# Kernel optimization log

Hardware: AMD Instinct MI355X
Metric: run time of the kernel (lower is better)

The kernel has to match this reference:

```python
import jax, jax.numpy as jnp
import numpy as np

B, T, C, H = 2, 2048, 1024, 16
HD = C // H  # 64

def setup_inputs() -> dict:
    key = jax.random.key(0)
    ks = jax.random.split(key, 9)
    s = 0.02
    return {
        "x": jax.random.normal(ks[0], (B, T, C), jnp.float32),
        "Wq": jax.random.normal(ks[1], (C, C), jnp.float32) * s,
        "bq": jax.random.normal(ks[2], (C,), jnp.float32) * s,
        "Wk": jax.random.normal(ks[3], (C, C), jnp.float32) * s,
        "bk": jax.random.normal(ks[4], (C,), jnp.float32) * s,
        "Wv": jax.random.normal(ks[5], (C, C), jnp.float32) * s,
        "bv": jax.random.normal(ks[6], (C,), jnp.float32) * s,
        "Wp": jax.random.normal(ks[7], (C, C), jnp.float32) * s,
        "bp": jax.random.normal(ks[8], (C,), jnp.float32) * s,
    }

def reference(x, Wq, bq, Wk, bk, Wv, bv, Wp, bp):
    Bb, Tt, Cc = x.shape
    hd = Cc // H
    # project and split heads: [B, H, T, hd]
    def heads(W, b):
        return (x @ W.T + b).reshape(Bb, Tt, H, hd).transpose(0, 2, 1, 3)
    q, k, v = heads(Wq, bq), heads(Wk, bk), heads(Wv, bv)
    scale = 1.0 / np.sqrt(hd).astype(np.float32)
    att = jnp.einsum('bhqd,bhkd->bhqk', q, k) * scale
    causal = jnp.tril(jnp.ones((Tt, Tt), bool))
    att = jnp.where(causal[None, None], att, -jnp.inf)
    att = jax.nn.softmax(att, axis=-1)
    y = jnp.einsum('bhqk,bhkd->bhqd', att, v)
    y = y.transpose(0, 2, 1, 3).reshape(Bb, Tt, Cc)
    return y @ Wp.T + bp
```

## Files before the change

kernel.cpp:

```cpp
#include <hip/hip_runtime.h>
#include <hip/hip_bf16.h>

#define Tsz 2048
#define Csz 1024
#define Hn 16

typedef short s8v __attribute__((ext_vector_type(8)));
typedef short s4v __attribute__((ext_vector_type(4)));
typedef float f4v __attribute__((ext_vector_type(4)));
typedef int   i4v __attribute__((ext_vector_type(4)));
typedef unsigned u2v __attribute__((ext_vector_type(2)));

#define QSCALE (0.125f * 1.44269504088896f)

__device__ __forceinline__ unsigned short bfr(float x) {
    return (unsigned short)((__builtin_bit_cast(unsigned, x) + 0x8000u) >> 16);
}
__device__ __forceinline__ unsigned pack2_rn(float a, float b) {
    const unsigned ua = __builtin_bit_cast(unsigned, a) + 0x8000u;
    const unsigned ub = __builtin_bit_cast(unsigned, b) + 0x8000u;
    return (ua >> 16) | (ub & 0xFFFF0000u);
}
__device__ __forceinline__ unsigned cvt2(float a, float b) {
    __hip_bfloat162 h = __float22bfloat162_rn(float2{a, b});
    unsigned r;
    __builtin_memcpy(&r, &h, 4);
    return r;
}

__device__ __forceinline__ void gload_lds(const void* g, void* l) {
    __builtin_amdgcn_global_load_lds(
        (const __attribute__((address_space(1))) void*)g,
        (__attribute__((address_space(3))) void*)l, 16, 0, 0);
}

__global__ void cvt6(const float* __restrict__ x, const float* __restrict__ wq,
                     const float* __restrict__ wk, const float* __restrict__ wv,
                     const float* __restrict__ wp,
                     short* __restrict__ xo, short* __restrict__ qo,
                     short* __restrict__ ko, short* __restrict__ vo,
                     short* __restrict__ po) {
    const int bx = blockIdx.x;
    const float* in; short* out; int ib;
    if (bx < 4096) { in = x; out = xo; ib = bx; }
    else {
        const int r = bx - 4096, w = r >> 10;
        ib = r & 1023;
        switch (w) {
            case 0: in = wq; out = qo; break;
            case 1: in = wk; out = ko; break;
            case 2: in = wv; out = vo; break;
            default: in = wp; out = po; break;
        }
    }
    const int i = ib * 1024 + threadIdx.x * 4;
    float4 v = *(const float4*)(in + i);
    int2 o;
    o.x = (int)pack2_rn(v.x, v.y);
    o.y = (int)pack2_rn(v.z, v.w);
    *(int2*)(out + i) = o;
}

__global__ __launch_bounds__(256, 3) void qkv_gemm(
    const short* __restrict__ X,
    const short* __restrict__ Wq, const short* __restrict__ Wk, const short* __restrict__ Wv,
    const float* __restrict__ bq, const float* __restrict__ bk, const float* __restrict__ bv,
    short* __restrict__ Qo, short* __restrict__ Ko, short* __restrict__ Vto)
{
    const int z = blockIdx.z;
    const short* W = (z == 0) ? Wq : (z == 1) ? Wk : Wv;
    const float* bias = (z == 0) ? bq : (z == 1) ? bk : bv;

    __shared__ __align__(16) short Ash[128 * 32];
    __shared__ __align__(16) short Bsh[128 * 32];
    __shared__ __align__(16) short TR[64 * 72];

    const int tid = threadIdx.x, lane = tid & 63, wave = tid >> 6;
    const int ln = lane & 15, hi = lane >> 4;
    const int m0 = blockIdx.x * 128, n0 = blockIdx.y * 128;
    const int wm = (wave >> 1) * 64, wn = (wave & 1) * 64;

    const short* Ag = X + (size_t)(m0 + (tid >> 2)) * Csz + (tid & 3) * 8;
    const short* Bg = W + (size_t)(n0 + (tid >> 2)) * Csz + (tid & 3) * 8;

    f4v acc[4][4];
    #pragma unroll
    for (int mt = 0; mt < 4; mt++)
        #pragma unroll
        for (int nt = 0; nt < 4; nt++)
            #pragma unroll
            for (int i = 0; i < 4; i++) acc[mt][nt][i] = 0.f;

    for (int k0 = 0; k0 < Csz; k0 += 32) {
        __syncthreads();
        gload_lds(Ag + k0, Ash + tid * 8);
        gload_lds(Ag + k0 + (size_t)64 * Csz, Ash + 2048 + tid * 8);
        gload_lds(Bg + k0, Bsh + tid * 8);
        gload_lds(Bg + k0 + (size_t)64 * Csz, Bsh + 2048 + tid * 8);
        __syncthreads();

        s8v af[4], bfr_[4];
        #pragma unroll
        for (int mt = 0; mt < 4; mt++)
            af[mt] = *(const s8v*)(Ash + (wm + mt * 16 + ln) * 32 + hi * 8);
        #pragma unroll
        for (int nt = 0; nt < 4; nt++)
            bfr_[nt] = *(const s8v*)(Bsh + (wn + nt * 16 + ln) * 32 + hi * 8);
        #pragma unroll
        for (int mt = 0; mt < 4; mt++)
            #pragma unroll
            for (int nt = 0; nt < 4; nt++)
                acc[mt][nt] = __builtin_amdgcn_mfma_f32_16x16x32_bf16(af[mt], bfr_[nt], acc[mt][nt], 0, 0, 0);
    }

    if (z == 2) {
        const int b = m0 >> 11, t0 = m0 & 2047;
        float bvv[4];
        #pragma unroll
        for (int nt = 0; nt < 4; nt++) bvv[nt] = bias[n0 + wn + nt * 16 + ln];
        #pragma unroll
        for (int ph = 0; ph < 4; ph++) {
            const int mh = ph >> 1, nh = ph & 1;
            __syncthreads();
            if ((wave >> 1) == mh && (wave & 1) == nh) {
                #pragma unroll
                for (int mt = 0; mt < 4; mt++)
                    #pragma unroll
                    for (int nt = 0; nt < 4; nt++) {
                        int2 pk;
                        pk.x = (int)pack2_rn(acc[mt][nt][0] + bvv[nt], acc[mt][nt][1] + bvv[nt]);
                        pk.y = (int)pack2_rn(acc[mt][nt][2] + bvv[nt], acc[mt][nt][3] + bvv[nt]);
                        *(int2*)(TR + (nt * 16 + ln) * 72 + mt * 16 + hi * 4) = pk;
                    }
            }
            __syncthreads();
            const int chl = tid >> 2, seg = tid & 3;
            const s8v r0 = *(const s8v*)(TR + chl * 72 + seg * 16);
            const s8v r1 = *(const s8v*)(TR + chl * 72 + seg * 16 + 8);
            short* dst = Vto + (size_t)(b * 1024 + n0 + nh * 64 + chl) * Tsz + t0 + mh * 64 + seg * 16;
            *(s8v*)(dst) = r0;
            *(s8v*)(dst + 8) = r1;
        }
        return;
    }

    const float scale = (z == 0) ? QSCALE : 1.0f;
    short* out = (z == 0) ? Qo : Ko;

    #pragma unroll
    for (int nt = 0; nt < 4; nt++) {
        const int col = n0 + wn + nt * 16 + ln;
        const float bvv = bias[col];
        #pragma unroll
        for (int mt = 0; mt < 4; mt++) {
            const int row0 = m0 + wm + mt * 16 + hi * 4;
            #pragma unroll
            for (int i = 0; i < 4; i++)
                out[(size_t)(row0 + i) * Csz + col] = (short)bfr((acc[mt][nt][i] + bvv) * scale);
        }
    }
}

__global__ __launch_bounds__(256, 2) void proj_gemm(
    const short* __restrict__ A, const short* __restrict__ W,
    const float* __restrict__ bias, float* __restrict__ out)
{
    __shared__ __align__(16) short Ash[128 * 32];
    __shared__ __align__(16) short Bsh[64 * 32];

    const int tid = threadIdx.x, lane = tid & 63, wave = tid >> 6;
    const int ln = lane & 15, hi = lane >> 4;
    const int m0 = blockIdx.x * 128, n0 = blockIdx.y * 64;
    const int wm = (wave >> 1) * 64, wn = (wave & 1) * 32;

    const short* Ag = A + (size_t)(m0 + (tid >> 2)) * Csz + (tid & 3) * 8;
    const short* Bg = W + (size_t)(n0 + (tid >> 2)) * Csz + (tid & 3) * 8;

    f4v acc[4][2];
    #pragma unroll
    for (int mt = 0; mt < 4; mt++)
        #pragma unroll
        for (int nt = 0; nt < 2; nt++)
            #pragma unroll
            for (int i = 0; i < 4; i++) acc[mt][nt][i] = 0.f;

    for (int k0 = 0; k0 < Csz; k0 += 32) {
        __syncthreads();
        gload_lds(Ag + k0, Ash + tid * 8);
        gload_lds(Ag + k0 + (size_t)64 * Csz, Ash + 2048 + tid * 8);
        gload_lds(Bg + k0, Bsh + tid * 8);
        __syncthreads();

        s8v af[4], bfr_[2];
        #pragma unroll
        for (int mt = 0; mt < 4; mt++)
            af[mt] = *(const s8v*)(Ash + (wm + mt * 16 + ln) * 32 + hi * 8);
        #pragma unroll
        for (int nt = 0; nt < 2; nt++)
            bfr_[nt] = *(const s8v*)(Bsh + (wn + nt * 16 + ln) * 32 + hi * 8);
        #pragma unroll
        for (int mt = 0; mt < 4; mt++)
            #pragma unroll
            for (int nt = 0; nt < 2; nt++)
                acc[mt][nt] = __builtin_amdgcn_mfma_f32_16x16x32_bf16(af[mt], bfr_[nt], acc[mt][nt], 0, 0, 0);
    }

    #pragma unroll
    for (int nt = 0; nt < 2; nt++) {
        const int col = n0 + wn + nt * 16 + ln;
        const float bvv = bias[col];
        #pragma unroll
        for (int mt = 0; mt < 4; mt++)
            #pragma unroll
            for (int i = 0; i < 4; i++)
                out[(size_t)(m0 + wm + mt * 16 + hi * 4 + i) * Csz + col] = acc[mt][nt][i] + bvv;
    }
}

__global__ __launch_bounds__(256, 3) void attn16(
    const short* __restrict__ Q, const short* __restrict__ Kg,
    const short* __restrict__ Vt, short* __restrict__ Y)
{
    __shared__ __align__(16) short SB[3][2][64 * 64];

    const int tid = threadIdx.x, lane = tid & 63, wave = tid >> 6;
    const int ln = lane & 15, hi = lane >> 4;

    const int n = blockIdx.x;
    const int c = n & 255, j = n >> 8;
    const int bh = (j << 3) | (c >> 5);
    const int t = c & 31;
    const int qt = (j & 1) ? t : 31 - t;

    const size_t base = (size_t)(bh >> 4) * Tsz * Csz + (size_t)(bh & 15) * 64;
    const size_t vtbase = (size_t)bh * 64 * Tsz;
    const int qrel = wave * 16 + ln;

    s8v qf[2];
    #pragma unroll
    for (int kk = 0; kk < 2; kk++)
        qf[kk] = *(const s8v*)(Q + base + (size_t)(qt * 64 + qrel) * Csz + kk * 32 + hi * 8);

    f4v o[4];
    f4v lacc;
    #pragma unroll
    for (int i = 0; i < 4; i++) lacc[i] = 0.f;
    #pragma unroll
    for (int dt = 0; dt < 4; dt++)
        #pragma unroll
        for (int i = 0; i < 4; i++) o[dt][i] = 0.f;

    const s8v ones8 = { (short)0x3F80, (short)0x3F80, (short)0x3F80, (short)0x3F80,
                        (short)0x3F80, (short)0x3F80, (short)0x3F80, (short)0x3F80 };

    const int sr = tid >> 3, scs = tid & 7;
    const int csw = (scs ^ (sr & 7)) * 8;
    const short* KsA = Kg + base + (size_t)sr * Csz + csw;
    const short* KsB = KsA + (size_t)32 * Csz;
    const short* VsA = Vt + vtbase + (size_t)sr * Tsz + csw;
    const short* VsB = VsA + (size_t)32 * Tsz;
    const int nkb = qt + 1;

    int foff[2][4];
    #pragma unroll
    for (int nt = 0; nt < 4; nt++)
        #pragma unroll
        for (int kk = 0; kk < 2; kk++)
            foff[kk][nt] = (nt * 16 + ln) * 64 + (((kk * 4 + hi) ^ (ln & 7)) * 8);

    #define STAGE3(B) {                                    \
        gload_lds(KsA, &SB[B][0][tid * 8]);                \
        gload_lds(KsB, &SB[B][0][2048 + tid * 8]);         \
        gload_lds(VsA, &SB[B][1][tid * 8]);                \
        gload_lds(VsB, &SB[B][1][2048 + tid * 8]);         \
        KsA += (size_t)64 * Csz; KsB += (size_t)64 * Csz;  \
        VsA += 64; VsB += 64;                              \
    }

    STAGE3(0);
    if (nkb > 1) {
        STAGE3(1);
        asm volatile("s_waitcnt vmcnt(4)" ::: "memory");
    } else {
        asm volatile("s_waitcnt vmcnt(0)" ::: "memory");
    }
    __builtin_amdgcn_s_barrier();

    #define TILE(B0, B2, kb_) {                                                     \
        const bool st_ = (kb_) + 2 < nkb;                                           \
        if (st_) STAGE3(B2);                                                        \
        s8v kf[2][4], vf[2][4];                                                     \
        for (int nt = 0; nt < 4; nt++) {                                            \
            kf[0][nt] = *(const s8v*)(&SB[B0][0][foff[0][nt]]);                     \
            kf[1][nt] = *(const s8v*)(&SB[B0][0][foff[1][nt]]);                     \
            vf[0][nt] = *(const s8v*)(&SB[B0][1][foff[0][nt]]);                     \
            vf[1][nt] = *(const s8v*)(&SB[B0][1][foff[1][nt]]);                     \
        }                                                                           \
        f4v s[4];                                                                   \
        for (int nt = 0; nt < 4; nt++) {                                            \
            for (int i = 0; i < 4; i++) s[nt][i] = 0.f;                             \
            s[nt] = __builtin_amdgcn_mfma_f32_16x16x32_bf16(kf[0][nt], qf[0], s[nt], 0, 0, 0); \
            s[nt] = __builtin_amdgcn_mfma_f32_16x16x32_bf16(kf[1][nt], qf[1], s[nt], 0, 0, 0); \
        }                                                                           \
        const bool dg_ = ((kb_) == qt);                                             \
        unsigned pw[4][2];                                                          \
        for (int nt = 0; nt < 4; nt++) {                                            \
            float e0 = exp2f(s[nt][0]), e1 = exp2f(s[nt][1]);                       \
            float e2 = exp2f(s[nt][2]), e3 = exp2f(s[nt][3]);                       \
            if (dg_) {                                                              \
                const int kr = nt * 16 + hi * 4;                                    \
                if (kr + 0 > qrel) e0 = 0.f;                                        \
                if (kr + 1 > qrel) e1 = 0.f;                                        \
                if (kr + 2 > qrel) e2 = 0.f;                                        \
                if (kr + 3 > qrel) e3 = 0.f;                                        \
            }                                                                       \
            pw[nt][0] = cvt2(e0, e1);                                               \
            pw[nt][1] = cvt2(e2, e3);                                               \
        }                                                                           \
        u2v r0a = __builtin_amdgcn_permlane32_swap(pw[0][0], pw[1][0], false, false); \
        u2v r0b = __builtin_amdgcn_permlane16_swap(r0a[0], r0a[1], false, false);   \
        u2v r1a = __builtin_amdgcn_permlane32_swap(pw[0][1], pw[1][1], false, false); \
        u2v r1b = __builtin_amdgcn_permlane16_swap(r1a[0], r1a[1], false, false);   \
        u2v r2a = __builtin_amdgcn_permlane32_swap(pw[2][0], pw[3][0], false, false); \
        u2v r2b = __builtin_amdgcn_permlane16_swap(r2a[0], r2a[1], false, false);   \
        u2v r3a = __builtin_amdgcn_permlane32_swap(pw[2][1], pw[3][1], false, false); \
        u2v r3b = __builtin_amdgcn_permlane16_swap(r3a[0], r3a[1], false, false);   \
        i4v p0 = { (int)r0b[0], (int)r1b[0], (int)r0b[1], (int)r1b[1] };            \
        i4v p1 = { (int)r2b[0], (int)r3b[0], (int)r2b[1], (int)r3b[1] };            \
        const s8v pb0 = __builtin_bit_cast(s8v, p0);                                \
        const s8v pb1 = __builtin_bit_cast(s8v, p1);                                \
        for (int dt = 0; dt < 4; dt++) {                                            \
            o[dt] = __builtin_amdgcn_mfma_f32_16x16x32_bf16(vf[0][dt], pb0, o[dt], 0, 0, 0); \
            o[dt] = __builtin_amdgcn_mfma_f32_16x16x32_bf16(vf[1][dt], pb1, o[dt], 0, 0, 0); \
        }                                                                           \
        lacc = __builtin_amdgcn_mfma_f32_16x16x32_bf16(ones8, pb0, lacc, 0, 0, 0);  \
        lacc = __builtin_amdgcn_mfma_f32_16x16x32_bf16(ones8, pb1, lacc, 0, 0, 0);  \
        if ((kb_) + 1 < nkb) {                                                      \
            if (st_) asm volatile("s_waitcnt vmcnt(4)" ::: "memory");               \
            else     asm volatile("s_waitcnt vmcnt(0)" ::: "memory");               \
            __builtin_amdgcn_s_barrier();                                           \
        }                                                                           \
    }

    for (int kb = 0; kb < nkb; kb += 3) {
        TILE(0, 2, kb);
        if (kb + 1 < nkb) TILE(1, 0, kb + 1);
        if (kb + 2 < nkb) TILE(2, 1, kb + 2);
    }
    #undef TILE
    #undef STAGE3

    const float inv = 1.0f / lacc[0];
    const int qrow = qt * 64 + qrel;
    #pragma unroll
    for (int dt = 0; dt < 4; dt++) {
        int2 w;
        w.x = (int)cvt2(o[dt][0] * inv, o[dt][1] * inv);
        w.y = (int)cvt2(o[dt][2] * inv, o[dt][3] * inv);
        *(int2*)(Y + base + (size_t)qrow * Csz + dt * 16 + hi * 4) = w;
    }
}

extern "C" void kernel_launch(void* const* d_in, const int* in_sizes, int n_in,
                              void* d_out, int out_size, void* d_ws, size_t ws_size,
                              hipStream_t stream) {
    const float* x  = (const float*)d_in[0];
    const float* Wq = (const float*)d_in[1];
    const float* bq = (const float*)d_in[2];
    const float* Wk = (const float*)d_in[3];
    const float* bk = (const float*)d_in[4];
    const float* Wv = (const float*)d_in[5];
    const float* bv = (const float*)d_in[6];
    const float* Wp = (const float*)d_in[7];
    const float* bp = (const float*)d_in[8];

    char* ws = (char*)d_ws;
    short* Xb  = (short*)(ws);
    short* Wqb = (short*)(ws + (8u  << 20));
    short* Wkb = (short*)(ws + (10u << 20));
    short* Wvb = (short*)(ws + (12u << 20));
    short* Wpb = (short*)(ws + (14u << 20));
    short* Qb  = (short*)(ws + (16u << 20));
    short* Kb  = (short*)(ws + (24u << 20));
    short* Vtb = (short*)(ws + (32u << 20));
    short* Yb  = (short*)(ws + (40u << 20));

    hipLaunchKernelGGL(cvt6, dim3(8192), dim3(256), 0, stream,
                       x, Wq, Wk, Wv, Wp, Xb, Wqb, Wkb, Wvb, Wpb);

    hipLaunchKernelGGL(qkv_gemm, dim3(32, 8, 3), dim3(256), 0, stream,
                       Xb, Wqb, Wkb, Wvb, bq, bk, bv, Qb, Kb, Vtb);

    hipLaunchKernelGGL(attn16, dim3(1024), dim3(256), 0, stream, Qb, Kb, Vtb, Yb);

    hipLaunchKernelGGL(proj_gemm, dim3(32, 16), dim3(256), 0, stream, Yb, Wpb, bp, (float*)d_out);
}
```

Baseline: 187.3 us.

## Pair causal query tiles per block to balance work and share K/V loads

Each attention block now handles two query tiles, t and 31-t, so every block processes the same 33 key tiles and shares each staged K/V tile between both queries. The grid drops from 1024 to 512 blocks. Pipelining goes from triple to double buffering with a full vmcnt(0) wait per tile, and launch bounds fall to 2 blocks per CU. This trades less prefetch depth, higher register pressure and lower occupancy for balanced work per block and fewer K/V loads.

New measurement: 178.8 us (median of 2 runs). 1.05x faster.

```diff
diff --git a/kernel.cpp b/kernel.cpp
--- a/kernel.cpp
+++ b/kernel.cpp
@@ -217,38 +217,44 @@
     }
 }
 
-__global__ __launch_bounds__(256, 3) void attn16(
+__global__ __launch_bounds__(256, 2) void attn17(
     const short* __restrict__ Q, const short* __restrict__ Kg,
     const short* __restrict__ Vt, short* __restrict__ Y)
 {
-    __shared__ __align__(16) short SB[3][2][64 * 64];
+    __shared__ __align__(16) short SB[2][2][64 * 64];
 
     const int tid = threadIdx.x, lane = tid & 63, wave = tid >> 6;
     const int ln = lane & 15, hi = lane >> 4;
 
     const int n = blockIdx.x;
-    const int c = n & 255, j = n >> 8;
-    const int bh = (j << 3) | (c >> 5);
-    const int t = c & 31;
-    const int qt = (j & 1) ? t : 31 - t;
+    const int j = n >> 8, n0 = n & 255;
+    const int bh = n0 >> 3, ti = n0 & 7;
+    const int t = j ? (15 - ti) : ti;
+    const int qts_[2] = { t, 31 - t };
+    const int nkb = 32 - t;
 
     const size_t base = (size_t)(bh >> 4) * Tsz * Csz + (size_t)(bh & 15) * 64;
     const size_t vtbase = (size_t)bh * 64 * Tsz;
     const int qrel = wave * 16 + ln;
 
-    s8v qf[2];
-    #pragma unroll
-    for (int kk = 0; kk < 2; kk++)
-        qf[kk] = *(const s8v*)(Q + base + (size_t)(qt * 64 + qrel) * Csz + kk * 32 + hi * 8);
-
-    f4v o[4];
-    f4v lacc;
-    #pragma unroll
-    for (int i = 0; i < 4; i++) lacc[i] = 0.f;
-    #pragma unroll
-    for (int dt = 0; dt < 4; dt++)
-        #pragma unroll
-        for (int i = 0; i < 4; i++) o[dt][i] = 0.f;
+    s8v qf[2][2];
+    #pragma unroll
+    for (int tt = 0; tt < 2; tt++)
+        #pragma unroll
+        for (int kk = 0; kk < 2; kk++)
+            qf[tt][kk] = *(const s8v*)(Q + base + (size_t)(qts_[tt] * 64 + qrel) * Csz + kk * 32 + hi * 8);
+
+    f4v o[2][4];
+    f4v lacc[2];
+    #pragma unroll
+    for (int tt = 0; tt < 2; tt++) {
+        #pragma unroll
+        for (int i = 0; i < 4; i++) lacc[tt][i] = 0.f;
+        #pragma unroll
+        for (int dt = 0; dt < 4; dt++)
+            #pragma unroll
+            for (int i = 0; i < 4; i++) o[tt][dt][i] = 0.f;
+    }
 
     const s8v ones8 = { (short)0x3F80, (short)0x3F80, (short)0x3F80, (short)0x3F80,
                         (short)0x3F80, (short)0x3F80, (short)0x3F80, (short)0x3F80 };
@@ -259,7 +265,6 @@
     const short* KsB = KsA + (size_t)32 * Csz;
     const short* VsA = Vt + vtbase + (size_t)sr * Tsz + csw;
     const short* VsB = VsA + (size_t)32 * Tsz;
-    const int nkb = qt + 1;
 
     int foff[2][4];
     #pragma unroll
@@ -268,27 +273,21 @@
         for (int kk = 0; kk < 2; kk++)
             foff[kk][nt] = (nt * 16 + ln) * 64 + (((kk * 4 + hi) ^ (ln & 7)) * 8);
 
-    #define STAGE3(B) {                                    \
-        gload_lds(KsA, &SB[B][0][tid * 8]);                \
-        gload_lds(KsB, &SB[B][0][2048 + tid * 8]);         \
-        gload_lds(VsA, &SB[B][1][tid * 8]);                \
-        gload_lds(VsB, &SB[B][1][2048 + tid * 8]);         \
-        KsA += (size_t)64 * Csz; KsB += (size_t)64 * Csz;  \
-        VsA += 64; VsB += 64;                              \
-    }
-
-    STAGE3(0);
-    if (nkb > 1) {
-        STAGE3(1);
-        asm volatile("s_waitcnt vmcnt(4)" ::: "memory");
-    } else {
-        asm volatile("s_waitcnt vmcnt(0)" ::: "memory");
-    }
+    #define STAGE(B, kb_) {                                      \
+        const size_t ko_ = (size_t)(kb_) * 64;                   \
+        gload_lds(KsA + ko_ * Csz, &SB[B][0][tid * 8]);          \
+        gload_lds(KsB + ko_ * Csz, &SB[B][0][2048 + tid * 8]);   \
+        gload_lds(VsA + ko_,       &SB[B][1][tid * 8]);          \
+        gload_lds(VsB + ko_,       &SB[B][1][2048 + tid * 8]);   \
+    }
+
+    STAGE(0, 0);
+    asm volatile("s_waitcnt vmcnt(0)" ::: "memory");
     __builtin_amdgcn_s_barrier();
 
-    #define TILE(B0, B2, kb_) {                                                     \
-        const bool st_ = (kb_) + 2 < nkb;                                           \
-        if (st_) STAGE3(B2);                                                        \
+    #define TILE(B0, B1, kb_) {                                                     \
+        const bool st_ = (kb_) + 1 < nkb;                                           \
+        if (st_) STAGE(B1, (kb_) + 1);                                              \
         s8v kf[2][4], vf[2][4];                                                     \
         for (int nt = 0; nt < 4; nt++) {                                            \
             kf[0][nt] = *(const s8v*)(&SB[B0][0][foff[0][nt]]);                     \
@@ -296,68 +295,73 @@
             vf[0][nt] = *(const s8v*)(&SB[B0][1][foff[0][nt]]);                     \
             vf[1][nt] = *(const s8v*)(&SB[B0][1][foff[1][nt]]);                     \
         }                                                                           \
-        f4v s[4];                                                                   \
-        for (int nt = 0; nt < 4; nt++) {                                            \
-            for (int i = 0; i < 4; i++) s[nt][i] = 0.f;                             \
-            s[nt] = __builtin_amdgcn_mfma_f32_16x16x32_bf16(kf[0][nt], qf[0], s[nt], 0, 0, 0); \
-            s[nt] = __builtin_amdgcn_mfma_f32_16x16x32_bf16(kf[1][nt], qf[1], s[nt], 0, 0, 0); \
+        _Pragma("unroll")                                                           \
+        for (int tt = 0; tt < 2; tt++) {                                            \
+            if ((kb_) > qts_[tt]) continue;                       \
+            f4v s[4];                                                               \
+            for (int nt = 0; nt < 4; nt++) {                                        \
+                for (int i = 0; i < 4; i++) s[nt][i] = 0.f;                         \
+                s[nt] = __builtin_amdgcn_mfma_f32_16x16x32_bf16(kf[0][nt], qf[tt][0], s[nt], 0, 0, 0); \
+                s[nt] = __builtin_amdgcn_mfma_f32_16x16x32_bf16(kf[1][nt], qf[tt][1], s[nt], 0, 0, 0); \
+            }                                                                       \
+            const bool dg_ = ((kb_) == qts_[tt]);                                   \
+            unsigned pw[4][2];                                                      \
+            for (int nt = 0; nt < 4; nt++) {                                        \
+                float e0 = exp2f(s[nt][0]), e1 = exp2f(s[nt][1]);                   \
+                float e2 = exp2f(s[nt][2]), e3 = exp2f(s[nt][3]);                   \
+                if (dg_) {                                                          \
+                    const int kr = nt * 16 + hi * 4;                                \
+                    if (kr + 0 > qrel) e0 = 0.f;                                    \
+                    if (kr + 1 > qrel) e1 = 0.f;                                    \
+                    if (kr + 2 > qrel) e2 = 0.f;                                    \
+                    if (kr + 3 > qrel) e3 = 0.f;                                    \
+                }                                                                   \
+                pw[nt][0] = cvt2(e0, e1);                                           \
+                pw[nt][1] = cvt2(e2, e3);                                           \
+            }                                                                       \
+            u2v r0a = __builtin_amdgcn_permlane32_swap(pw[0][0], pw[1][0], false, false); \
+            u2v r0b = __builtin_amdgcn_permlane16_swap(r0a[0], r0a[1], false, false); \
+            u2v r1a = __builtin_amdgcn_permlane32_swap(pw[0][1], pw[1][1], false, false); \
+            u2v r1b = __builtin_amdgcn_permlane16_swap(r1a[0], r1a[1], false, false); \
+            u2v r2a = __builtin_amdgcn_permlane32_swap(pw[2][0], pw[3][0], false, false); \
+            u2v r2b = __builtin_amdgcn_permlane16_swap(r2a[0], r2a[1], false, false); \
+            u2v r3a = __builtin_amdgcn_permlane32_swap(pw[2][1], pw[3][1], false, false); \
+            u2v r3b = __builtin_amdgcn_permlane16_swap(r3a[0], r3a[1], false, false); \
+            i4v p0 = { (int)r0b[0], (int)r1b[0], (int)r0b[1], (int)r1b[1] };        \
+            i4v p1 = { (int)r2b[0], (int)r3b[0], (int)r2b[1], (int)r3b[1] };        \
+            const s8v pb0 = __builtin_bit_cast(s8v, p0);                            \
+            const s8v pb1 = __builtin_bit_cast(s8v, p1);                            \
+            for (int dt = 0; dt < 4; dt++) {                                        \
+                o[tt][dt] = __builtin_amdgcn_mfma_f32_16x16x32_bf16(vf[0][dt], pb0, o[tt][dt], 0, 0, 0); \
+                o[tt][dt] = __builtin_amdgcn_mfma_f32_16x16x32_bf16(vf[1][dt], pb1, o[tt][dt], 0, 0, 0); \
+            }                                                                       \
+            lacc[tt] = __builtin_amdgcn_mfma_f32_16x16x32_bf16(ones8, pb0, lacc[tt], 0, 0, 0); \
+            lacc[tt] = __builtin_amdgcn_mfma_f32_16x16x32_bf16(ones8, pb1, lacc[tt], 0, 0, 0); \
         }                                                                           \
-        const bool dg_ = ((kb_) == qt);                                             \
-        unsigned pw[4][2];                                                          \
-        for (int nt = 0; nt < 4; nt++) {                                            \
-            float e0 = exp2f(s[nt][0]), e1 = exp2f(s[nt][1]);                       \
-            float e2 = exp2f(s[nt][2]), e3 = exp2f(s[nt][3]);                       \
-            if (dg_) {                                                              \
-                const int kr = nt * 16 + hi * 4;                                    \
-                if (kr + 0 > qrel) e0 = 0.f;                                        \
-                if (kr + 1 > qrel) e1 = 0.f;                                        \
-                if (kr + 2 > qrel) e2 = 0.f;                                        \
-                if (kr + 3 > qrel) e3 = 0.f;                                        \
-            }                                                                       \
-            pw[nt][0] = cvt2(e0, e1);                                               \
-            pw[nt][1] = cvt2(e2, e3);                                               \
-        }                                                                           \
-        u2v r0a = __builtin_amdgcn_permlane32_swap(pw[0][0], pw[1][0], false, false); \
-        u2v r0b = __builtin_amdgcn_permlane16_swap(r0a[0], r0a[1], false, false);   \
-        u2v r1a = __builtin_amdgcn_permlane32_swap(pw[0][1], pw[1][1], false, false); \
-        u2v r1b = __builtin_amdgcn_permlane16_swap(r1a[0], r1a[1], false, false);   \
-        u2v r2a = __builtin_amdgcn_permlane32_swap(pw[2][0], pw[3][0], false, false); \
-        u2v r2b = __builtin_amdgcn_permlane16_swap(r2a[0], r2a[1], false, false);   \
-        u2v r3a = __builtin_amdgcn_permlane32_swap(pw[2][1], pw[3][1], false, false); \
-        u2v r3b = __builtin_amdgcn_permlane16_swap(r3a[0], r3a[1], false, false);   \
-        i4v p0 = { (int)r0b[0], (int)r1b[0], (int)r0b[1], (int)r1b[1] };            \
-        i4v p1 = { (int)r2b[0], (int)r3b[0], (int)r2b[1], (int)r3b[1] };            \
-        const s8v pb0 = __builtin_bit_cast(s8v, p0);                                \
-        const s8v pb1 = __builtin_bit_cast(s8v, p1);                                \
-        for (int dt = 0; dt < 4; dt++) {                                            \
-            o[dt] = __builtin_amdgcn_mfma_f32_16x16x32_bf16(vf[0][dt], pb0, o[dt], 0, 0, 0); \
-            o[dt] = __builtin_amdgcn_mfma_f32_16x16x32_bf16(vf[1][dt], pb1, o[dt], 0, 0, 0); \
-        }                                                                           \
-        lacc = __builtin_amdgcn_mfma_f32_16x16x32_bf16(ones8, pb0, lacc, 0, 0, 0);  \
-        lacc = __builtin_amdgcn_mfma_f32_16x16x32_bf16(ones8, pb1, lacc, 0, 0, 0);  \
-        if ((kb_) + 1 < nkb) {                                                      \
-            if (st_) asm volatile("s_waitcnt vmcnt(4)" ::: "memory");               \
-            else     asm volatile("s_waitcnt vmcnt(0)" ::: "memory");               \
+        if (st_) {                                                                  \
+            asm volatile("s_waitcnt vmcnt(0)" ::: "memory");                        \
             __builtin_amdgcn_s_barrier();                                           \
         }                                                                           \
     }
 
-    for (int kb = 0; kb < nkb; kb += 3) {
-        TILE(0, 2, kb);
+    for (int kb = 0; kb < nkb; kb += 2) {
+        TILE(0, 1, kb);
         if (kb + 1 < nkb) TILE(1, 0, kb + 1);
-        if (kb + 2 < nkb) TILE(2, 1, kb + 2);
     }
     #undef TILE
-    #undef STAGE3
-
-    const float inv = 1.0f / lacc[0];
-    const int qrow = qt * 64 + qrel;
-    #pragma unroll
-    for (int dt = 0; dt < 4; dt++) {
-        int2 w;
-        w.x = (int)cvt2(o[dt][0] * inv, o[dt][1] * inv);
-        w.y = (int)cvt2(o[dt][2] * inv, o[dt][3] * inv);
-        *(int2*)(Y + base + (size_t)qrow * Csz + dt * 16 + hi * 4) = w;
+    #undef STAGE
+
+    #pragma unroll
+    for (int tt = 0; tt < 2; tt++) {
+        const float inv = 1.0f / lacc[tt][0];
+        const int qrow = qts_[tt] * 64 + qrel;
+        #pragma unroll
+        for (int dt = 0; dt < 4; dt++) {
+            int2 w;
+            w.x = (int)cvt2(o[tt][dt][0] * inv, o[tt][dt][1] * inv);
+            w.y = (int)cvt2(o[tt][dt][2] * inv, o[tt][dt][3] * inv);
+            *(int2*)(Y + base + (size_t)qrow * Csz + dt * 16 + hi * 4) = w;
+        }
     }
 }
 
@@ -391,7 +395,7 @@
     hipLaunchKernelGGL(qkv_gemm, dim3(32, 8, 3), dim3(256), 0, stream,
                        Xb, Wqb, Wkb, Wvb, bq, bk, bv, Qb, Kb, Vtb);
 
-    hipLaunchKernelGGL(attn16, dim3(1024), dim3(256), 0, stream, Qb, Kb, Vtb, Yb);
+    hipLaunchKernelGGL(attn17, dim3(512), dim3(256), 0, stream, Qb, Kb, Vtb, Yb);
 
     hipLaunchKernelGGL(proj_gemm, dim3(32, 16), dim3(256), 0, stream, Yb, Wpb, bp, (float*)d_out);
 }
```
